# Performance work log

Measured on AMD Instinct MI355X. Metric: run time of the kernel, lower is better.

Reference implementation:

```python
import jax, jax.numpy as jnp
import numpy as np

B, M, Q, D = 32, 8192, 64, 128

def setup_inputs() -> dict:
    key = jax.random.key(0)
    k1, k2, k3, k4 = jax.random.split(key, 4)
    story_a = jax.random.normal(k1, (B, M, D), dtype=jnp.float32)
    u = jax.random.normal(k2, (B, Q, D), dtype=jnp.float32)
    story_c = jax.random.normal(k3, (B, M, D), dtype=jnp.float32)
    H = jax.random.normal(k4, (D, D), dtype=jnp.float32) * (1.0 / np.sqrt(D))
    return {"story_a": story_a, "u": u, "story_c": story_c, "H": H}

def reference(story_a, u, story_c, H):
    # scores: Dot(axes=-1)([story_a, u]) -> (B, M, Q)
    m = jnp.einsum('bmd,bqd->bmq', story_a, u)
    # Keras Softmax() default axis=-1: normalize over Q (faithful to original)
    p = jax.nn.softmax(m, axis=-1)          # (B, M, Q)
    p = jnp.swapaxes(p, 1, 2)                # (B, Q, M)
    # output memory: Dot(axes=(2,1))([p, story_c]) -> (B, Q, D)
    c = jnp.einsum('bqm,bmd->bqd', p, story_c)
    # linear residual: K.dot(u, H) + c
    mapped_u = jnp.einsum('bqd,de->bqe', u, H)
    return c + mapped_u
```

## Files before the change

kernel.cpp:

```cpp
#include <hip/hip_runtime.h>

#define B_ 32
#define M_ 8192
#define Q_ 64
#define D_ 128
#define MT 64
#define LDP 72
#define LDCP 260

typedef __attribute__((ext_vector_type(8))) short short8;
typedef __attribute__((ext_vector_type(4))) float floatx4;

__device__ __forceinline__ unsigned pkbf(float a, float b) {
  unsigned ua = __builtin_bit_cast(unsigned, a) + 0x8000u;
  unsigned ub = __builtin_bit_cast(unsigned, b) + 0x8000u;
  return __builtin_amdgcn_perm(ub, ua, 0x07060302u);
}

__device__ __forceinline__ short8 pack8(float4 a, float4 b) {
  union { unsigned u[4]; short8 v; } o;
  o.u[0] = pkbf(a.x, a.y); o.u[1] = pkbf(a.z, a.w);
  o.u[2] = pkbf(b.x, b.y); o.u[3] = pkbf(b.z, b.w);
  return o.v;
}

template <int CTRL>
__device__ __forceinline__ float dppadd(float x) {
  int y = __builtin_amdgcn_update_dpp(0, __builtin_bit_cast(int, x), CTRL, 0xF, 0xF, true);
  return x + __builtin_bit_cast(float, y);
}
__device__ __forceinline__ float rowsum16(float x) {
  x = dppadd<0x128>(x); x = dppadd<0x124>(x);
  x = dppadd<0x122>(x); x = dppadd<0x121>(x);
  return x;
}

__device__ __forceinline__ void barrier_lds() {
  asm volatile("s_waitcnt lgkmcnt(0)\n\ts_barrier" ::: "memory");
}

__device__ __forceinline__ void dma16(const float* g, float* l) {
  __builtin_amdgcn_global_load_lds(
      (const __attribute__((address_space(1))) void*)g,
      (__attribute__((address_space(3))) void*)l, 16, 0, 0);
}

template <int NT, bool ATOMIC>
__global__ __launch_bounds__(256, 2) void memn2n_main(
    const float* __restrict__ A, const float* __restrict__ U,
    const float* __restrict__ Cc, float* __restrict__ dst) {
  __shared__ __align__(16) float sCb[2][32 * LDCP];
  __shared__ __align__(16) unsigned short sP[Q_ * LDP];

  const int tid  = threadIdx.x;
  const int lane = tid & 63;
  const int w    = tid >> 6;
  const int l15  = lane & 15;
  const int quad = (lane >> 4) & 3;

  constexpr int chunks = (M_ / MT) / NT;
  const int blk = blockIdx.x;
  const int b   = blk / chunks;
  const int ch  = blk - b * chunks;

  const float* Abase = A + ((size_t)b * M_ + (size_t)ch * NT * MT) * D_;
  const float* Cbase = Cc + ((size_t)b * M_ + (size_t)ch * NT * MT) * D_;

  const float* ub = U + (size_t)b * Q_ * D_;
  short8 uf[4][4];
#pragma unroll
  for (int qs = 0; qs < 4; ++qs)
#pragma unroll
    for (int ks = 0; ks < 4; ++ks) {
      const float* p = ub + (16 * qs + l15) * D_ + 32 * ks + 8 * quad;
      uf[qs][ks] = pack8(*(const float4*)p, *(const float4*)(p + 4));
    }

  float4 pA[2][8];

#define DMA_TILE(tt, bi)                                                        \
  {                                                                             \
    const float* Ct_ = Cbase + (size_t)(tt) * MT * D_;                          \
    _Pragma("unroll") for (int j = 0; j < 8; ++j) {                             \
      int p = w * 8 + j;                                                        \
      dma16(Ct_ + p * 256 + (lane >> 5) * 128 + (lane & 31) * 4,                \
            &sCb[bi][p * LDCP]);                                                \
    }                                                                           \
  }
#define LOAD_A(tt, bi)                                                          \
  {                                                                             \
    const float* Ar_ = Abase + (size_t)(tt) * MT * D_ + (16 * w + l15) * D_ + 8 * quad; \
    _Pragma("unroll") for (int ks = 0; ks < 4; ++ks) {                          \
      pA[bi][2 * ks]     = *(const float4*)(Ar_ + 32 * ks);                     \
      pA[bi][2 * ks + 1] = *(const float4*)(Ar_ + 32 * ks + 4);                 \
    }                                                                           \
  }

  DMA_TILE(0, 0);
  LOAD_A(0, 0);

  floatx4 acc[2][4];
#pragma unroll
  for (int i = 0; i < 2; ++i)
#pragma unroll
    for (int j = 0; j < 4; ++j) acc[i][j] = (floatx4){0.f, 0.f, 0.f, 0.f};

#pragma unroll
  for (int t = 0; t < NT; ++t) {
    const int cur = t & 1, nxt = cur ^ 1;

    floatx4 s1[4];
#pragma unroll
    for (int qs = 0; qs < 4; ++qs) s1[qs] = (floatx4){0.f, 0.f, 0.f, 0.f};
#pragma unroll
    for (int ks = 0; ks < 4; ++ks) {
      short8 af = pack8(pA[cur][2 * ks], pA[cur][2 * ks + 1]);
#pragma unroll
      for (int qs = 0; qs < 4; ++qs)
        s1[qs] = __builtin_amdgcn_mfma_f32_16x16x32_bf16(af, uf[qs][ks], s1[qs], 0, 0, 0);
    }

    float pv[4][4];
#pragma unroll
    for (int rg = 0; rg < 4; ++rg) {
      const float c = 1.4426950408889634f;
      float e0 = exp2f(s1[0][rg] * c), e1 = exp2f(s1[1][rg] * c);
      float e2 = exp2f(s1[2][rg] * c), e3 = exp2f(s1[3][rg] * c);
      float sm = (e0 + e1) + (e2 + e3);
      sm = rowsum16(sm);
      float inv = __builtin_amdgcn_rcpf(sm);
      pv[0][rg] = e0 * inv; pv[1][rg] = e1 * inv;
      pv[2][rg] = e2 * inv; pv[3][rg] = e3 * inv;
    }

    barrier_lds();

    if (t + 1 < NT) {
      DMA_TILE(t + 1, nxt);
      LOAD_A(t + 1, nxt);
    }

#pragma unroll
    for (int qs = 0; qs < 4; ++qs)
      *(uint2*)&sP[(16 * qs + l15) * LDP + 16 * w + 4 * quad] =
          make_uint2(pkbf(pv[qs][0], pv[qs][1]), pkbf(pv[qs][2], pv[qs][3]));

    barrier_lds();

#pragma unroll
    for (int ks = 0; ks < 2; ++ks) {
      short8 pa[4];
#pragma unroll
      for (int qs = 0; qs < 4; ++qs)
        pa[qs] = *(const short8*)&sP[(16 * qs + l15) * LDP + 32 * ks + 8 * quad];
#pragma unroll
      for (int ds = 0; ds < 2; ++ds) {
        int d = l15 + 16 * (2 * w + ds);
        float cc[8];
#pragma unroll
        for (int j = 0; j < 8; ++j)
          cc[j] = sCb[cur][(16 * ks + 4 * quad + (j >> 1)) * LDCP + (j & 1) * 128 + d];
        union { unsigned u[4]; short8 v; } o;
        o.u[0] = pkbf(cc[0], cc[1]); o.u[1] = pkbf(cc[2], cc[3]);
        o.u[2] = pkbf(cc[4], cc[5]); o.u[3] = pkbf(cc[6], cc[7]);
#pragma unroll
        for (int qs = 0; qs < 4; ++qs)
          acc[ds][qs] = __builtin_amdgcn_mfma_f32_16x16x32_bf16(pa[qs], o.v, acc[ds][qs], 0, 0, 0);
      }
    }
  }

  if (ATOMIC) {
#pragma unroll
    for (int ds = 0; ds < 2; ++ds)
#pragma unroll
      for (int qs = 0; qs < 4; ++qs)
#pragma unroll
        for (int rg = 0; rg < 4; ++rg) {
          int q = qs * 16 + quad * 4 + rg;
          int d = l15 + 16 * (2 * w + ds);
          atomicAdd(&dst[((size_t)b * Q_ + q) * D_ + d], acc[ds][qs][rg]);
        }
  } else {
    float* pp = dst + (((size_t)ch * B_ + b) * Q_) * D_;
#pragma unroll
    for (int ds = 0; ds < 2; ++ds)
#pragma unroll
      for (int qs = 0; qs < 4; ++qs)
#pragma unroll
        for (int rg = 0; rg < 4; ++rg) {
          int q = qs * 16 + quad * 4 + rg;
          int d = l15 + 16 * (2 * w + ds);
          pp[q * D_ + d] = acc[ds][qs][rg];
        }
  }
#undef DMA_TILE
#undef LOAD_A
}

__global__ __launch_bounds__(128) void memn2n_reduce(
    const float* __restrict__ U, const float* __restrict__ H,
    const float* __restrict__ part, float* __restrict__ out, int chunks) {
  int bq = blockIdx.x;
  int b = bq >> 6, q = bq & 63;
  int d = threadIdx.x;
  __shared__ float su[D_];
  size_t row = ((size_t)b * Q_ + q) * D_;
  su[d] = U[row + d];
  __syncthreads();
  float acc = 0.f;
#pragma unroll 16
  for (int e = 0; e < D_; ++e) acc = fmaf(su[e], H[e * D_ + d], acc);
#pragma unroll 8
  for (int ch = 0; ch < chunks; ++ch)
    acc += part[(((size_t)ch * B_ + b) * Q_ + q) * D_ + d];
  out[row + d] = acc;
}

extern "C" void kernel_launch(void* const* d_in, const int* in_sizes, int n_in,
                              void* d_out, int out_size, void* d_ws, size_t ws_size,
                              hipStream_t stream) {
  const float* A  = (const float*)d_in[0];
  const float* U  = (const float*)d_in[1];
  const float* Cc = (const float*)d_in[2];
  const float* H  = (const float*)d_in[3];
  float* out = (float*)d_out;

  const int CHn = 16;
  size_t part_bytes = (size_t)CHn * B_ * Q_ * D_ * sizeof(float);
  if (ws_size >= part_bytes) {
    float* part = (float*)d_ws;
    memn2n_main<8, false><<<B_ * CHn, 256, 0, stream>>>(A, U, Cc, part);
    memn2n_reduce<<<B_ * Q_, 128, 0, stream>>>(U, H, part, out, CHn);
  } else {
    memn2n_reduce<<<B_ * Q_, 128, 0, stream>>>(U, H, nullptr, out, 0);
    memn2n_main<16, true><<<B_ * 8, 256, 0, stream>>>(A, U, Cc, out);
  }
}
```

Baseline: 297.1 us.

## Stream A and C tiles into wave-private LDS via async DMA with one barrier

Each wave now uses global_load_lds to DMA its own A rows and its own C column slice into a private double-buffered LDS region, replacing register-staged A loads and the shared C buffer. The P tile is double-buffered, which drops one of the two barriers per tile, and waits use explicit vmcnt counts. The grid is halved to one 256-thread block per CU with twice as many tiles per block, and the launch bound drops to one block per CU. This aims to cut register pressure and synchronisation stalls, at the cost of fewer resident waves to hide memory latency and a much larger LDS footprint.

New measurement: 296.1 us. No clear change (-0.3%).

```diff
diff --git a/kernel.cpp b/kernel.cpp
--- a/kernel.cpp
+++ b/kernel.cpp
@@ -5,8 +5,14 @@
 #define Q_ 64
 #define D_ 128
 #define MT 64
+#define NT 16
+#define CHN 8
 #define LDP 72
-#define LDCP 260
+#define SA 268
+#define SC 260
+#define AW (8 * SA)
+#define CW (8 * SC)
+#define WBUF (AW + CW)
 
 typedef __attribute__((ext_vector_type(8))) short short8;
 typedef __attribute__((ext_vector_type(4))) float floatx4;
@@ -45,12 +51,12 @@
       (__attribute__((address_space(3))) void*)l, 16, 0, 0);
 }
 
-template <int NT, bool ATOMIC>
-__global__ __launch_bounds__(256, 2) void memn2n_main(
+template <bool ATOMIC>
+__global__ __launch_bounds__(256, 1) void memn2n_main(
     const float* __restrict__ A, const float* __restrict__ U,
     const float* __restrict__ Cc, float* __restrict__ dst) {
-  __shared__ __align__(16) float sCb[2][32 * LDCP];
-  __shared__ __align__(16) unsigned short sP[Q_ * LDP];
+  __shared__ __align__(16) float sMem[4 * 2 * WBUF];
+  __shared__ __align__(16) unsigned short sP[2][Q_ * LDP];
 
   const int tid  = threadIdx.x;
   const int lane = tid & 63;
@@ -58,13 +64,14 @@
   const int l15  = lane & 15;
   const int quad = (lane >> 4) & 3;
 
-  constexpr int chunks = (M_ / MT) / NT;
   const int blk = blockIdx.x;
-  const int b   = blk / chunks;
-  const int ch  = blk - b * chunks;
+  const int b   = blk / CHN;
+  const int ch  = blk - b * CHN;
 
   const float* Abase = A + ((size_t)b * M_ + (size_t)ch * NT * MT) * D_;
   const float* Cbase = Cc + ((size_t)b * M_ + (size_t)ch * NT * MT) * D_;
+
+  float* const wbase = sMem + w * (2 * WBUF);
 
   const float* ub = U + (size_t)b * Q_ * D_;
   short8 uf[4][4];
@@ -76,28 +83,17 @@
       uf[qs][ks] = pack8(*(const float4*)p, *(const float4*)(p + 4));
     }
 
-  float4 pA[2][8];
-
-#define DMA_TILE(tt, bi)                                                        \
-  {                                                                             \
-    const float* Ct_ = Cbase + (size_t)(tt) * MT * D_;                          \
-    _Pragma("unroll") for (int j = 0; j < 8; ++j) {                             \
-      int p = w * 8 + j;                                                        \
-      dma16(Ct_ + p * 256 + (lane >> 5) * 128 + (lane & 31) * 4,                \
-            &sCb[bi][p * LDCP]);                                                \
-    }                                                                           \
-  }
-#define LOAD_A(tt, bi)                                                          \
-  {                                                                             \
-    const float* Ar_ = Abase + (size_t)(tt) * MT * D_ + (16 * w + l15) * D_ + 8 * quad; \
-    _Pragma("unroll") for (int ks = 0; ks < 4; ++ks) {                          \
-      pA[bi][2 * ks]     = *(const float4*)(Ar_ + 32 * ks);                     \
-      pA[bi][2 * ks + 1] = *(const float4*)(Ar_ + 32 * ks + 4);                 \
-    }                                                                           \
-  }
-
-  DMA_TILE(0, 0);
-  LOAD_A(0, 0);
+#define DMA_TILE(tt, bufp)                                                       \
+  {                                                                              \
+    const float* At_ = Abase + ((size_t)(tt) * MT + 16 * w) * D_;                \
+    const float* Ct_ = Cbase + (size_t)(tt) * MT * D_ + 32 * w;                  \
+    float* dA_ = (bufp);                                                         \
+    float* dC_ = (bufp) + AW;                                                    \
+    _Pragma("unroll") for (int j = 0; j < 8; ++j)                                \
+      dma16(At_ + j * 256 + lane * 4, dA_ + j * SA);                             \
+    _Pragma("unroll") for (int j = 0; j < 8; ++j)                                \
+      dma16(Ct_ + (8 * j + (lane >> 3)) * D_ + (lane & 7) * 4, dC_ + j * SC);    \
+  }
 
   floatx4 acc[2][4];
 #pragma unroll
@@ -105,19 +101,33 @@
 #pragma unroll
     for (int j = 0; j < 4; ++j) acc[i][j] = (floatx4){0.f, 0.f, 0.f, 0.f};
 
-#pragma unroll
+  DMA_TILE(0, wbase);
+
   for (int t = 0; t < NT; ++t) {
-    const int cur = t & 1, nxt = cur ^ 1;
+    float* buf = wbase + (t & 1) * WBUF;
+
+    if (t + 1 < NT) {
+      float* nbuf = wbase + ((t + 1) & 1) * WBUF;
+      DMA_TILE(t + 1, nbuf);
+      asm volatile("s_waitcnt vmcnt(16)" ::: "memory");
+    } else {
+      asm volatile("s_waitcnt vmcnt(0)" ::: "memory");
+    }
 
     floatx4 s1[4];
 #pragma unroll
     for (int qs = 0; qs < 4; ++qs) s1[qs] = (floatx4){0.f, 0.f, 0.f, 0.f};
-#pragma unroll
-    for (int ks = 0; ks < 4; ++ks) {
-      short8 af = pack8(pA[cur][2 * ks], pA[cur][2 * ks + 1]);
-#pragma unroll
-      for (int qs = 0; qs < 4; ++qs)
-        s1[qs] = __builtin_amdgcn_mfma_f32_16x16x32_bf16(af, uf[qs][ks], s1[qs], 0, 0, 0);
+    {
+      const int rb = (l15 >> 1) * SA + (l15 & 1) * 128 + 8 * quad;
+#pragma unroll
+      for (int ks = 0; ks < 4; ++ks) {
+        float4 x = *(const float4*)(buf + rb + 32 * ks);
+        float4 y = *(const float4*)(buf + rb + 32 * ks + 4);
+        short8 af = pack8(x, y);
+#pragma unroll
+        for (int qs = 0; qs < 4; ++qs)
+          s1[qs] = __builtin_amdgcn_mfma_f32_16x16x32_bf16(af, uf[qs][ks], s1[qs], 0, 0, 0);
+      }
     }
 
     float pv[4][4];
@@ -133,33 +143,27 @@
       pv[2][rg] = e2 * inv; pv[3][rg] = e3 * inv;
     }
 
+    unsigned short* sPt = &sP[t & 1][0];
+#pragma unroll
+    for (int qs = 0; qs < 4; ++qs)
+      *(uint2*)&sPt[(16 * qs + l15) * LDP + 16 * w + 4 * quad] =
+          make_uint2(pkbf(pv[qs][0], pv[qs][1]), pkbf(pv[qs][2], pv[qs][3]));
+
     barrier_lds();
 
-    if (t + 1 < NT) {
-      DMA_TILE(t + 1, nxt);
-      LOAD_A(t + 1, nxt);
-    }
-
-#pragma unroll
-    for (int qs = 0; qs < 4; ++qs)
-      *(uint2*)&sP[(16 * qs + l15) * LDP + 16 * w + 4 * quad] =
-          make_uint2(pkbf(pv[qs][0], pv[qs][1]), pkbf(pv[qs][2], pv[qs][3]));
-
-    barrier_lds();
-
+    const float* aC = buf + AW;
 #pragma unroll
     for (int ks = 0; ks < 2; ++ks) {
       short8 pa[4];
 #pragma unroll
       for (int qs = 0; qs < 4; ++qs)
-        pa[qs] = *(const short8*)&sP[(16 * qs + l15) * LDP + 32 * ks + 8 * quad];
+        pa[qs] = *(const short8*)&sPt[(16 * qs + l15) * LDP + 32 * ks + 8 * quad];
 #pragma unroll
       for (int ds = 0; ds < 2; ++ds) {
-        int d = l15 + 16 * (2 * w + ds);
         float cc[8];
 #pragma unroll
         for (int j = 0; j < 8; ++j)
-          cc[j] = sCb[cur][(16 * ks + 4 * quad + (j >> 1)) * LDCP + (j & 1) * 128 + d];
+          cc[j] = aC[(4 * ks + quad) * SC + j * 32 + 16 * ds + l15];
         union { unsigned u[4]; short8 v; } o;
         o.u[0] = pkbf(cc[0], cc[1]); o.u[1] = pkbf(cc[2], cc[3]);
         o.u[2] = pkbf(cc[4], cc[5]); o.u[3] = pkbf(cc[6], cc[7]);
@@ -195,7 +199,6 @@
         }
   }
 #undef DMA_TILE
-#undef LOAD_A
 }
 
 __global__ __launch_bounds__(128) void memn2n_reduce(
@@ -226,14 +229,13 @@
   const float* H  = (const float*)d_in[3];
   float* out = (float*)d_out;
 
-  const int CHn = 16;
-  size_t part_bytes = (size_t)CHn * B_ * Q_ * D_ * sizeof(float);
+  size_t part_bytes = (size_t)CHN * B_ * Q_ * D_ * sizeof(float);
   if (ws_size >= part_bytes) {
     float* part = (float*)d_ws;
-    memn2n_main<8, false><<<B_ * CHn, 256, 0, stream>>>(A, U, Cc, part);
-    memn2n_reduce<<<B_ * Q_, 128, 0, stream>>>(U, H, part, out, CHn);
+    memn2n_main<false><<<B_ * CHN, 256, 0, stream>>>(A, U, Cc, part);
+    memn2n_reduce<<<B_ * Q_, 128, 0, stream>>>(U, H, part, out, CHN);
   } else {
     memn2n_reduce<<<B_ * Q_, 128, 0, stream>>>(U, H, nullptr, out, 0);
-    memn2n_main<16, true><<<B_ * 8, 256, 0, stream>>>(A, U, Cc, out);
-  }
-}
+    memn2n_main<true><<<B_ * CHN, 256, 0, stream>>>(A, U, Cc, out);
+  }
+}
```
